# Kernel tuning notes

Measured on AMD Instinct MI355X. Metric: run time of the kernel, lower is better.

## Reference

```python
import jax, jax.numpy as jnp
import numpy as np

NHEAD = 4
HEAD_DIM = 64  # att_features per head = atten_feats // nhead


def setup_inputs() -> dict:
    key = jax.random.key(0)
    ks = jax.random.split(key, 8)
    N, D = 8192, 256
    s = 1.0 / np.sqrt(D)
    return {
        "x": jax.random.normal(ks[0], (N, D), dtype=jnp.float32),
        "edge": jax.random.randint(ks[1], (N, N), 0, 2, dtype=jnp.int32),
        "Wq": jax.random.normal(ks[2], (D, D), dtype=jnp.float32) * s,
        "bq": jax.random.normal(ks[3], (D,), dtype=jnp.float32) * 0.01,
        "Wk": jax.random.normal(ks[4], (D, D), dtype=jnp.float32) * s,
        "bk": jax.random.normal(ks[5], (D,), dtype=jnp.float32) * 0.01,
        "Wv": jax.random.normal(ks[6], (D, D), dtype=jnp.float32) * s,
        "bv": jax.random.normal(ks[7], (D,), dtype=jnp.float32) * 0.01,
    }


def _split_heads(t):
    # (N, H*d) -> (H, N, d)
    N = t.shape[0]
    return t.reshape(N, NHEAD, HEAD_DIM).transpose(1, 0, 2)


def reference(x, edge, Wq, bq, Wk, bk, Wv, bv):
    q = _split_heads(x @ Wq + bq)  # (H, N, d)
    k = _split_heads(x @ Wk + bk)
    v = _split_heads(x @ Wv + bv)
    # additive graph mask: 0 where edge.T == 1, -10000 where edge.T == 0
    mask = (edge.T.astype(jnp.float32) - 1.0) * 10000.0  # (N, N)
    scores = jnp.einsum("hnd,hmd->hnm", q, k) / np.sqrt(HEAD_DIM)
    scores = scores + mask[None, :, :]
    attn = jax.nn.softmax(scores, axis=-1)  # dropout is identity at eval
    ctx = jnp.einsum("hnm,hmd->hnd", attn, v)
    # (H, N, d) -> (N, H*d)
    return ctx.transpose(1, 0, 2).reshape(x.shape[0], NHEAD * HEAD_DIM)
```

## Files before the change

### kernel.cpp

```cpp
#include <hip/hip_runtime.h>
#include <stdint.h>

typedef unsigned short u16;
typedef unsigned int u32;
typedef unsigned long long u64;

typedef __attribute__((ext_vector_type(8))) __bf16 bf16x8;
typedef __attribute__((ext_vector_type(4))) float f32x4;

#define NROW 8192
#define DMODEL 256
#define HD 64
#define LDT 72

__device__ __forceinline__ u16 f2bf(float f) {
    u32 u = __builtin_bit_cast(u32, f);
    u += 0x7FFFu + ((u >> 16) & 1u);
    return (u16)(u >> 16);
}
__device__ __forceinline__ bf16x8 ldb8(const u16* p) {
    uint4 v = *(const uint4*)p;
    return __builtin_bit_cast(bf16x8, v);
}
__device__ __forceinline__ f32x4 mfma16(bf16x8 a, bf16x8 b, f32x4 c) {
    return __builtin_amdgcn_mfma_f32_16x16x32_bf16(a, b, c, 0, 0, 0);
}

__global__ __launch_bounds__(256) void k_prep(
    const float* __restrict__ x,
    const float* __restrict__ Wq, const float* __restrict__ Wk,
    const float* __restrict__ Wv,
    u16* __restrict__ xb, u16* __restrict__ Wt) {
    const int t = threadIdx.x;
    if (blockIdx.x < 1024) {
        size_t idx = (size_t)blockIdx.x * 2048 + t * 8;
        f32x4 a = *(const f32x4*)&x[idx];
        f32x4 b = *(const f32x4*)&x[idx + 4];
        uint4 o;
        o.x = (u32)f2bf(a[0]) | ((u32)f2bf(a[1]) << 16);
        o.y = (u32)f2bf(a[2]) | ((u32)f2bf(a[3]) << 16);
        o.z = (u32)f2bf(b[0]) | ((u32)f2bf(b[1]) << 16);
        o.w = (u32)f2bf(b[2]) | ((u32)f2bf(b[3]) << 16);
        *(uint4*)&xb[idx] = o;
        return;
    }
    __shared__ __align__(16) u16 lw[64 * LDT];
    int wb = blockIdx.x - 1024;
    int mat = wb >> 4, tile = wb & 15;
    int k0 = (tile >> 2) * 64, n0 = (tile & 3) * 64;
    const float* W = (mat == 0) ? Wq : ((mat == 1) ? Wk : Wv);
    #pragma unroll
    for (int i = 0; i < 4; ++i) {
        int c = t + 256 * i;
        int k = c >> 4, c4 = c & 15;
        f32x4 w4 = *(const f32x4*)&W[(size_t)(k0 + k) * DMODEL + n0 + c4 * 4];
        uint2 pk;
        pk.x = (u32)f2bf(w4[0]) | ((u32)f2bf(w4[1]) << 16);
        pk.y = (u32)f2bf(w4[2]) | ((u32)f2bf(w4[3]) << 16);
        *(uint2*)&lw[k * LDT + c4 * 4] = pk;
    }
    __syncthreads();
    #pragma unroll
    for (int i = 0; i < 2; ++i) {
        int c = t + 256 * i;
        int n = c >> 3, k8 = c & 7;
        union { uint4 u; u16 s[8]; } pk;
        #pragma unroll
        for (int j = 0; j < 8; ++j) pk.s[j] = lw[(k8 * 8 + j) * LDT + n];
        *(uint4*)&Wt[(size_t)mat * 65536 + (size_t)(n0 + n) * DMODEL + k0 + k8 * 8] = pk.u;
    }
}

__global__ __launch_bounds__(256) void k_bitmask(const int* __restrict__ edge,
                                                 u64* __restrict__ bits) {
    __shared__ u64 lb[8][128];
    const int t = threadIdx.x;
    const int lane = t & 63, w = t >> 6;
    const u32 m8 = blockIdx.x * 8u;
    #pragma unroll
    for (int rr = 0; rr < 2; ++rr) {
        const int mloc = w * 2 + rr;
        const size_t base = (size_t)(m8 + mloc) * NROW;
        for (int nwb = 0; nwb < 128; nwb += 16) {
            int v[16];
            #pragma unroll
            for (int j = 0; j < 16; ++j)
                v[j] = edge[base + (size_t)(nwb + j) * 64 + lane];
            u64 b[16];
            #pragma unroll
            for (int j = 0; j < 16; ++j) b[j] = __ballot(v[j] != 0);
            if (lane == 0) {
                #pragma unroll
                for (int j = 0; j < 16; ++j) lb[mloc][nwb + j] = b[j];
            }
        }
    }
    __syncthreads();
    const int nw = t >> 1, mh = (t & 1) * 4;
    u64 a0 = lb[mh + 0][nw], a1 = lb[mh + 1][nw];
    u64 a2 = lb[mh + 2][nw], a3 = lb[mh + 3][nw];
    u64* dst = &bits[(size_t)nw * NROW + m8 + mh];
    uint4 p0, p1;
    p0.x = (u32)a0; p0.y = (u32)(a0 >> 32); p0.z = (u32)a1; p0.w = (u32)(a1 >> 32);
    p1.x = (u32)a2; p1.y = (u32)(a2 >> 32); p1.z = (u32)a3; p1.w = (u32)(a3 >> 32);
    *(uint4*)dst = p0;
    *(uint4*)(dst + 2) = p1;
}

__global__ __launch_bounds__(256, 3) void k_qkv(
    const u16* __restrict__ xb, const u16* __restrict__ Wt,
    const float* __restrict__ bq, const float* __restrict__ bk,
    const float* __restrict__ bv,
    u16* __restrict__ Qo, u16* __restrict__ Ko, u16* __restrict__ Vt) {
    __shared__ __align__(16) u16 ax[128 * LDT];
    __shared__ __align__(16) u16 wt[64 * LDT];
    const int t = threadIdx.x;
    const int lane = t & 63, wv = t >> 6;
    const int q4 = lane >> 4, l15 = lane & 15;
    const int wr = wv >> 1, wc = wv & 1;
    const int row0 = blockIdx.x * 128;
    const int mat = blockIdx.y >> 2;
    const int c0 = (blockIdx.y & 3) * 64;
    const u16* Wm = Wt + (size_t)mat * 65536;
    const float* bias = (mat == 0) ? bq : ((mat == 1) ? bk : bv);

    f32x4 acc[8];
    #pragma unroll
    for (int i = 0; i < 8; ++i) acc[i] = {0.f, 0.f, 0.f, 0.f};

    for (int kk = 0; kk < DMODEL; kk += 64) {
        #pragma unroll
        for (int i = 0; i < 4; ++i) {
            int c = t + 256 * i;
            int row = c >> 3, c8 = c & 7;
            *(uint4*)&ax[row * LDT + c8 * 8] =
                *(const uint4*)&xb[(size_t)(row0 + row) * DMODEL + kk + c8 * 8];
        }
        #pragma unroll
        for (int i = 0; i < 2; ++i) {
            int c = t + 256 * i;
            int n = c >> 3, c8 = c & 7;
            *(uint4*)&wt[n * LDT + c8 * 8] =
                *(const uint4*)&Wm[(size_t)(c0 + n) * DMODEL + kk + c8 * 8];
        }
        __syncthreads();
        #pragma unroll
        for (int ks = 0; ks < 2; ++ks) {
            bf16x8 xf[4], wf[2];
            #pragma unroll
            for (int it = 0; it < 4; ++it)
                xf[it] = ldb8(&ax[(wr * 64 + it * 16 + l15) * LDT + ks * 32 + q4 * 8]);
            #pragma unroll
            for (int jt = 0; jt < 2; ++jt)
                wf[jt] = ldb8(&wt[(wc * 32 + jt * 16 + l15) * LDT + ks * 32 + q4 * 8]);
            if (mat < 2) {
                #pragma unroll
                for (int it = 0; it < 4; ++it)
                    #pragma unroll
                    for (int jt = 0; jt < 2; ++jt)
                        acc[it * 2 + jt] = mfma16(xf[it], wf[jt], acc[it * 2 + jt]);
            } else {
                #pragma unroll
                for (int jt = 0; jt < 2; ++jt)
                    #pragma unroll
                    for (int it = 0; it < 4; ++it)
                        acc[jt * 4 + it] = mfma16(wf[jt], xf[it], acc[jt * 4 + it]);
            }
        }
        __syncthreads();
    }

    if (mat < 2) {
        u16* out = (mat == 0) ? Qo : Ko;
        const float scale = (mat == 0) ? 0.18033688f : 1.0f;
        #pragma unroll
        for (int jt = 0; jt < 2; ++jt) {
            int col = c0 + wc * 32 + jt * 16 + l15;
            float bcol = bias[col];
            #pragma unroll
            for (int it = 0; it < 4; ++it) {
                int rowb = row0 + wr * 64 + it * 16 + q4 * 4;
                f32x4 a = acc[it * 2 + jt];
                #pragma unroll
                for (int r = 0; r < 4; ++r)
                    out[(size_t)(rowb + r) * DMODEL + col] = f2bf((a[r] + bcol) * scale);
            }
        }
    } else {
        #pragma unroll
        for (int jt = 0; jt < 2; ++jt) {
            #pragma unroll
            for (int r = 0; r < 4; ++r) {
                int drow = c0 + wc * 32 + jt * 16 + q4 * 4 + r;
                float bd = bias[drow];
                #pragma unroll
                for (int it = 0; it < 4; ++it) {
                    int col = row0 + wr * 64 + it * 16 + l15;
                    Vt[(size_t)drow * NROW + col] = f2bf(acc[jt * 4 + it][r] + bd);
                }
            }
        }
    }
}

__global__ __launch_bounds__(256, 2) void k_attn(
    const u16* __restrict__ Q, const u16* __restrict__ K,
    const u16* __restrict__ Vt, const u64* __restrict__ bits,
    float* __restrict__ po) {
    __shared__ __align__(16) u16 sK[2][64 * 64];
    __shared__ __align__(16) u16 sV[2][64 * 64];
    __shared__ __align__(16) u16 sP[4][16 * 64];
    __shared__ __align__(16) u32 sB[2][2][64];

    const int t = threadIdx.x;
    const int lane = t & 63, w = t >> 6;
    const int q4 = lane >> 4, l15 = lane & 15;
    const int l7 = l15 & 7;
    const int bid = blockIdx.x;
    const int sl = bid >> 9;
    const int b9 = bid & 511;
    const int h = (b9 >> 1) & 3;
    const int qt = ((b9 >> 3) << 1) | (b9 & 1);
    const int n0 = qt * 64;
    const int mbase = sl * 2048;
    const int half = w >> 1;
    const u32 shift = (u32)((w & 1) * 16 + l15);
    const int sr = t >> 3, sc = t & 7;
    const int ssw = (sc ^ (sr & 7)) * 8;

    bf16x8 qf[2];
    #pragma unroll
    for (int ks = 0; ks < 2; ++ks)
        qf[ks] = ldb8(&Q[(size_t)(n0 + w * 16 + l15) * DMODEL + h * HD + ks * 32 + q4 * 8]);

    uint4 onesu = {0x3F803F80u, 0x3F803F80u, 0x3F803F80u, 0x3F803F80u};
    const bf16x8 ones = __builtin_bit_cast(bf16x8, onesu);

    f32x4 o[4], lacc;
    lacc = {0.f, 0.f, 0.f, 0.f};
    #pragma unroll
    for (int dt = 0; dt < 4; ++dt) o[dt] = {0.f, 0.f, 0.f, 0.f};

    uint4 rk0, rk1, rv0, rv1; uint2 rb;
    {
        rk0 = *(const uint4*)&K[(size_t)(mbase + sr) * DMODEL + h * HD + sc * 8];
        rk1 = *(const uint4*)&K[(size_t)(mbase + 32 + sr) * DMODEL + h * HD + sc * 8];
        rv0 = *(const uint4*)&Vt[(size_t)(h * HD + sr) * NROW + mbase + sc * 8];
        rv1 = *(const uint4*)&Vt[(size_t)(h * HD + 32 + sr) * NROW + mbase + sc * 8];
        if (t < 64) rb = *(const uint2*)&bits[(size_t)qt * NROW + mbase + t];
        *(uint4*)&sK[0][sr * 64 + ssw] = rk0;
        *(uint4*)&sK[0][(32 + sr) * 64 + ssw] = rk1;
        *(uint4*)&sV[0][sr * 64 + ssw] = rv0;
        *(uint4*)&sV[0][(32 + sr) * 64 + ssw] = rv1;
        if (t < 64) { sB[0][0][t] = rb.x; sB[0][1][t] = rb.y; }
    }

    for (int it = 0; it < 32; ++it) {
        __syncthreads();
        const int buf = it & 1;
        if (it < 31) {
            int m0 = mbase + (it + 1) * 64;
            rk0 = *(const uint4*)&K[(size_t)(m0 + sr) * DMODEL + h * HD + sc * 8];
            rk1 = *(const uint4*)&K[(size_t)(m0 + 32 + sr) * DMODEL + h * HD + sc * 8];
            rv0 = *(const uint4*)&Vt[(size_t)(h * HD + sr) * NROW + m0 + sc * 8];
            rv1 = *(const uint4*)&Vt[(size_t)(h * HD + 32 + sr) * NROW + m0 + sc * 8];
            if (t < 64) rb = *(const uint2*)&bits[(size_t)qt * NROW + m0 + t];
        }

        f32x4 s[4];
        #pragma unroll
        for (int tj = 0; tj < 4; ++tj) s[tj] = {0.f, 0.f, 0.f, 0.f};
        #pragma unroll
        for (int ks = 0; ks < 2; ++ks) {
            bf16x8 kb[4];
            #pragma unroll
            for (int tj = 0; tj < 4; ++tj)
                kb[tj] = ldb8(&sK[buf][(tj * 16 + l15) * 64 + (((ks * 4 + q4) ^ l7) * 8)]);
            #pragma unroll
            for (int tj = 0; tj < 4; ++tj)
                s[tj] = mfma16(kb[tj], qf[ks], s[tj]);
        }

        #pragma unroll
        for (int tj = 0; tj < 4; ++tj) {
            uint4 bw = *(const uint4*)&sB[buf][half][tj * 16 + q4 * 4];
            u32 wd[4] = {bw.x, bw.y, bw.z, bw.w};
            u32 ub[4];
            #pragma unroll
            for (int r = 0; r < 4; ++r) {
                float sv = ((wd[r] >> shift) & 1u) ? s[tj][r] : -1e30f;
                ub[r] = __builtin_bit_cast(u32, __builtin_amdgcn_exp2f(sv));
            }
            uint2 pk;
            pk.x = (ub[0] >> 16) | (ub[1] & 0xFFFF0000u);
            pk.y = (ub[2] >> 16) | (ub[3] & 0xFFFF0000u);
            *(uint2*)&sP[w][l15 * 64 + (((tj * 2 + (q4 >> 1)) ^ l7) * 8) + (q4 & 1) * 4] = pk;
        }
        asm volatile("s_waitcnt lgkmcnt(0)" ::: "memory");

        #pragma unroll
        for (int ks = 0; ks < 2; ++ks) {
            bf16x8 pf = ldb8(&sP[w][l15 * 64 + (((ks * 4 + q4) ^ l7) * 8)]);
            bf16x8 vb[4];
            #pragma unroll
            for (int dt = 0; dt < 4; ++dt)
                vb[dt] = ldb8(&sV[buf][(dt * 16 + l15) * 64 + (((ks * 4 + q4) ^ l7) * 8)]);
            #pragma unroll
            for (int dt = 0; dt < 4; ++dt)
                o[dt] = mfma16(pf, vb[dt], o[dt]);
            lacc = mfma16(pf, ones, lacc);
        }

        if (it < 31) {
            const int nb = buf ^ 1;
            *(uint4*)&sK[nb][sr * 64 + ssw] = rk0;
            *(uint4*)&sK[nb][(32 + sr) * 64 + ssw] = rk1;
            *(uint4*)&sV[nb][sr * 64 + ssw] = rv0;
            *(uint4*)&sV[nb][(32 + sr) * 64 + ssw] = rv1;
            if (t < 64) { sB[nb][0][t] = rb.x; sB[nb][1][t] = rb.y; }
        }
    }

    float* pob = po + (size_t)bid * 4160;
    #pragma unroll
    for (int dt = 0; dt < 4; ++dt)
        *(f32x4*)&pob[(dt * 16 + l15) * 64 + w * 16 + q4 * 4] = o[dt];
    if (l15 == 0) {
        #pragma unroll
        for (int r = 0; r < 4; ++r) pob[4096 + w * 16 + q4 * 4 + r] = lacc[r];
    }
}

__global__ __launch_bounds__(256) void k_reduce(const float* __restrict__ po,
                                                float* __restrict__ out) {
    __shared__ float sT[64 * 68];
    __shared__ float sL[64];
    const int t = threadIdx.x;
    const int b9 = blockIdx.x;
    const int h = (b9 >> 1) & 3;
    const int qt = ((b9 >> 3) << 1) | (b9 & 1);
    const int n0 = qt * 64;
    const size_t base = (size_t)b9 * 4160;
    const int d = t >> 2, ng = (t & 3) * 16;
    f32x4 a[4];
    #pragma unroll
    for (int j = 0; j < 4; ++j) a[j] = {0.f, 0.f, 0.f, 0.f};
    #pragma unroll
    for (int s = 0; s < 4; ++s) {
        const float* p = po + base + (size_t)s * (512 * 4160) + d * 64 + ng;
        #pragma unroll
        for (int j = 0; j < 4; ++j) a[j] += *(const f32x4*)&p[j * 4];
    }
    #pragma unroll
    for (int j = 0; j < 4; ++j) *(f32x4*)&sT[d * 68 + ng + j * 4] = a[j];
    if (t < 64) {
        float l = 0.f;
        #pragma unroll
        for (int s = 0; s < 4; ++s) l += po[base + (size_t)s * (512 * 4160) + 4096 + t];
        sL[t] = l;
    }
    __syncthreads();
    const int n = t >> 2, dg = (t & 3) * 16;
    float inv = __builtin_amdgcn_rcpf(sL[n] + 1e-30f);
    #pragma unroll
    for (int j = 0; j < 4; ++j) {
        f32x4 v;
        #pragma unroll
        for (int i = 0; i < 4; ++i) v[i] = sT[(dg + j * 4 + i) * 68 + n];
        v = v * inv;
        *(f32x4*)&out[(size_t)(n0 + n) * DMODEL + h * HD + dg + j * 4] = v;
    }
}

extern "C" void kernel_launch(void* const* d_in, const int* in_sizes, int n_in,
                              void* d_out, int out_size, void* d_ws, size_t ws_size,
                              hipStream_t stream) {
    const float* x  = (const float*)d_in[0];
    const int* edge = (const int*)d_in[1];
    const float* Wq = (const float*)d_in[2];
    const float* bq = (const float*)d_in[3];
    const float* Wk = (const float*)d_in[4];
    const float* bk = (const float*)d_in[5];
    const float* Wv = (const float*)d_in[6];
    const float* bv = (const float*)d_in[7];

    char* ws = (char*)d_ws;
    u64* bits = (u64*)ws;
    u16* Qo  = (u16*)(ws + (8u << 20));
    u16* Ko  = (u16*)(ws + (12u << 20));
    u16* Vt  = (u16*)(ws + (16u << 20));
    u16* xb  = (u16*)(ws + (20u << 20));
    u16* Wt  = (u16*)(ws + (24u << 20));
    float* po = (float*)(ws + (32u << 20));
    float* out = (float*)d_out;

    hipLaunchKernelGGL(k_prep, dim3(1072), dim3(256), 0, stream, x, Wq, Wk, Wv, xb, Wt);
    hipLaunchKernelGGL(k_bitmask, dim3(1024), dim3(256), 0, stream, edge, bits);
    hipLaunchKernelGGL(k_qkv, dim3(64, 12), dim3(256), 0, stream,
                       xb, Wt, bq, bk, bv, Qo, Ko, Vt);
    hipLaunchKernelGGL(k_attn, dim3(2048), dim3(256), 0, stream, Qo, Ko, Vt, bits, po);
    hipLaunchKernelGGL(k_reduce, dim3(512), dim3(256), 0, stream, po, out);
}
```

Before: 514.4 us.

## Process two query tiles per attention block to reuse K/V tiles

Each attention block now handles 128 query rows (two 64-row tiles) per head and key slice, so every K and V tile staged in shared memory feeds twice as many MFMAs. The grid drops to 1024 attention blocks and 256 reduce blocks, and the partial-output layout and reduce kernel are adapted to match. The aim is to halve K/V global and LDS traffic per unit of work. In exchange it roughly doubles accumulator and score registers and enlarges the P buffer in shared memory, which may limit occupancy even with launch bounds raised to 3.

```diff
diff --git a/kernel.cpp b/kernel.cpp
--- a/kernel.cpp
+++ b/kernel.cpp
@@ -203,43 +203,50 @@
     }
 }
 
-__global__ __launch_bounds__(256, 2) void k_attn(
+__global__ __launch_bounds__(256, 3) void k_attn(
     const u16* __restrict__ Q, const u16* __restrict__ K,
     const u16* __restrict__ Vt, const u64* __restrict__ bits,
     float* __restrict__ po) {
     __shared__ __align__(16) u16 sK[2][64 * 64];
     __shared__ __align__(16) u16 sV[2][64 * 64];
-    __shared__ __align__(16) u16 sP[4][16 * 64];
-    __shared__ __align__(16) u32 sB[2][2][64];
+    __shared__ __align__(16) u16 sP[4][32 * 64];
+    __shared__ __align__(16) u32 sB[2][2][2][64];
 
     const int t = threadIdx.x;
     const int lane = t & 63, w = t >> 6;
     const int q4 = lane >> 4, l15 = lane & 15;
     const int l7 = l15 & 7;
     const int bid = blockIdx.x;
-    const int sl = bid >> 9;
-    const int b9 = bid & 511;
-    const int h = (b9 >> 1) & 3;
-    const int qt = ((b9 >> 3) << 1) | (b9 & 1);
-    const int n0 = qt * 64;
+    const int sl = bid >> 8;
+    const int b8 = bid & 255;
+    const int h = b8 & 3;
+    const int qt = b8 >> 2;
+    const int n0 = qt * 128;
     const int mbase = sl * 2048;
     const int half = w >> 1;
     const u32 shift = (u32)((w & 1) * 16 + l15);
     const int sr = t >> 3, sc = t & 7;
     const int ssw = (sc ^ (sr & 7)) * 8;
-
-    bf16x8 qf[2];
-    #pragma unroll
-    for (int ks = 0; ks < 2; ++ks)
-        qf[ks] = ldb8(&Q[(size_t)(n0 + w * 16 + l15) * DMODEL + h * HD + ks * 32 + q4 * 8]);
+    const int bg = t >> 6, bm = t & 63;
+
+    bf16x8 qf[2][2];
+    #pragma unroll
+    for (int nt = 0; nt < 2; ++nt)
+        #pragma unroll
+        for (int ks = 0; ks < 2; ++ks)
+            qf[nt][ks] = ldb8(&Q[(size_t)(n0 + nt * 64 + w * 16 + l15) * DMODEL +
+                                 h * HD + ks * 32 + q4 * 8]);
 
     uint4 onesu = {0x3F803F80u, 0x3F803F80u, 0x3F803F80u, 0x3F803F80u};
     const bf16x8 ones = __builtin_bit_cast(bf16x8, onesu);
 
-    f32x4 o[4], lacc;
-    lacc = {0.f, 0.f, 0.f, 0.f};
-    #pragma unroll
-    for (int dt = 0; dt < 4; ++dt) o[dt] = {0.f, 0.f, 0.f, 0.f};
+    f32x4 o[2][4], lacc[2];
+    #pragma unroll
+    for (int nt = 0; nt < 2; ++nt) {
+        lacc[nt] = {0.f, 0.f, 0.f, 0.f};
+        #pragma unroll
+        for (int dt = 0; dt < 4; ++dt) o[nt][dt] = {0.f, 0.f, 0.f, 0.f};
+    }
 
     uint4 rk0, rk1, rv0, rv1; uint2 rb;
     {
@@ -247,12 +254,12 @@
         rk1 = *(const uint4*)&K[(size_t)(mbase + 32 + sr) * DMODEL + h * HD + sc * 8];
         rv0 = *(const uint4*)&Vt[(size_t)(h * HD + sr) * NROW + mbase + sc * 8];
         rv1 = *(const uint4*)&Vt[(size_t)(h * HD + 32 + sr) * NROW + mbase + sc * 8];
-        if (t < 64) rb = *(const uint2*)&bits[(size_t)qt * NROW + mbase + t];
+        if (t < 128) rb = *(const uint2*)&bits[(size_t)(qt * 2 + bg) * NROW + mbase + bm];
         *(uint4*)&sK[0][sr * 64 + ssw] = rk0;
         *(uint4*)&sK[0][(32 + sr) * 64 + ssw] = rk1;
         *(uint4*)&sV[0][sr * 64 + ssw] = rv0;
         *(uint4*)&sV[0][(32 + sr) * 64 + ssw] = rv1;
-        if (t < 64) { sB[0][0][t] = rb.x; sB[0][1][t] = rb.y; }
+        if (t < 128) { sB[0][bg][0][bm] = rb.x; sB[0][bg][1][bm] = rb.y; }
     }
 
     for (int it = 0; it < 32; ++it) {
@@ -264,12 +271,14 @@
             rk1 = *(const uint4*)&K[(size_t)(m0 + 32 + sr) * DMODEL + h * HD + sc * 8];
             rv0 = *(const uint4*)&Vt[(size_t)(h * HD + sr) * NROW + m0 + sc * 8];
             rv1 = *(const uint4*)&Vt[(size_t)(h * HD + 32 + sr) * NROW + m0 + sc * 8];
-            if (t < 64) rb = *(const uint2*)&bits[(size_t)qt * NROW + m0 + t];
-        }
-
-        f32x4 s[4];
-        #pragma unroll
-        for (int tj = 0; tj < 4; ++tj) s[tj] = {0.f, 0.f, 0.f, 0.f};
+            if (t < 128) rb = *(const uint2*)&bits[(size_t)(qt * 2 + bg) * NROW + m0 + bm];
+        }
+
+        f32x4 s[2][4];
+        #pragma unroll
+        for (int nt = 0; nt < 2; ++nt)
+            #pragma unroll
+            for (int tj = 0; tj < 4; ++tj) s[nt][tj] = {0.f, 0.f, 0.f, 0.f};
         #pragma unroll
         for (int ks = 0; ks < 2; ++ks) {
             bf16x8 kb[4];
@@ -277,38 +286,49 @@
             for (int tj = 0; tj < 4; ++tj)
                 kb[tj] = ldb8(&sK[buf][(tj * 16 + l15) * 64 + (((ks * 4 + q4) ^ l7) * 8)]);
             #pragma unroll
-            for (int tj = 0; tj < 4; ++tj)
-                s[tj] = mfma16(kb[tj], qf[ks], s[tj]);
-        }
-
-        #pragma unroll
-        for (int tj = 0; tj < 4; ++tj) {
-            uint4 bw = *(const uint4*)&sB[buf][half][tj * 16 + q4 * 4];
-            u32 wd[4] = {bw.x, bw.y, bw.z, bw.w};
-            u32 ub[4];
-            #pragma unroll
-            for (int r = 0; r < 4; ++r) {
-                float sv = ((wd[r] >> shift) & 1u) ? s[tj][r] : -1e30f;
-                ub[r] = __builtin_bit_cast(u32, __builtin_amdgcn_exp2f(sv));
-            }
-            uint2 pk;
-            pk.x = (ub[0] >> 16) | (ub[1] & 0xFFFF0000u);
-            pk.y = (ub[2] >> 16) | (ub[3] & 0xFFFF0000u);
-            *(uint2*)&sP[w][l15 * 64 + (((tj * 2 + (q4 >> 1)) ^ l7) * 8) + (q4 & 1) * 4] = pk;
+            for (int nt = 0; nt < 2; ++nt)
+                #pragma unroll
+                for (int tj = 0; tj < 4; ++tj)
+                    s[nt][tj] = mfma16(kb[tj], qf[nt][ks], s[nt][tj]);
+        }
+
+        #pragma unroll
+        for (int nt = 0; nt < 2; ++nt) {
+            #pragma unroll
+            for (int tj = 0; tj < 4; ++tj) {
+                uint4 bw = *(const uint4*)&sB[buf][nt][half][tj * 16 + q4 * 4];
+                u32 wd[4] = {bw.x, bw.y, bw.z, bw.w};
+                u32 ub[4];
+                #pragma unroll
+                for (int r = 0; r < 4; ++r) {
+                    float sv = ((wd[r] >> shift) & 1u) ? s[nt][tj][r] : -1e30f;
+                    ub[r] = __builtin_bit_cast(u32, __builtin_amdgcn_exp2f(sv));
+                }
+                uint2 pk;
+                pk.x = (ub[0] >> 16) | (ub[1] & 0xFFFF0000u);
+                pk.y = (ub[2] >> 16) | (ub[3] & 0xFFFF0000u);
+                *(uint2*)&sP[w][(nt * 16 + l15) * 64 +
+                                (((tj * 2 + (q4 >> 1)) ^ l7) * 8) + (q4 & 1) * 4] = pk;
+            }
         }
         asm volatile("s_waitcnt lgkmcnt(0)" ::: "memory");
 
         #pragma unroll
         for (int ks = 0; ks < 2; ++ks) {
-            bf16x8 pf = ldb8(&sP[w][l15 * 64 + (((ks * 4 + q4) ^ l7) * 8)]);
-            bf16x8 vb[4];
+            bf16x8 pf[2], vb[4];
+            #pragma unroll
+            for (int nt = 0; nt < 2; ++nt)
+                pf[nt] = ldb8(&sP[w][(nt * 16 + l15) * 64 + (((ks * 4 + q4) ^ l7) * 8)]);
             #pragma unroll
             for (int dt = 0; dt < 4; ++dt)
                 vb[dt] = ldb8(&sV[buf][(dt * 16 + l15) * 64 + (((ks * 4 + q4) ^ l7) * 8)]);
             #pragma unroll
-            for (int dt = 0; dt < 4; ++dt)
-                o[dt] = mfma16(pf, vb[dt], o[dt]);
-            lacc = mfma16(pf, ones, lacc);
+            for (int nt = 0; nt < 2; ++nt) {
+                #pragma unroll
+                for (int dt = 0; dt < 4; ++dt)
+                    o[nt][dt] = mfma16(pf[nt], vb[dt], o[nt][dt]);
+                lacc[nt] = mfma16(pf[nt], ones, lacc[nt]);
+            }
         }
 
         if (it < 31) {
@@ -317,56 +337,61 @@
             *(uint4*)&sK[nb][(32 + sr) * 64 + ssw] = rk1;
             *(uint4*)&sV[nb][sr * 64 + ssw] = rv0;
             *(uint4*)&sV[nb][(32 + sr) * 64 + ssw] = rv1;
-            if (t < 64) { sB[nb][0][t] = rb.x; sB[nb][1][t] = rb.y; }
-        }
-    }
-
-    float* pob = po + (size_t)bid * 4160;
-    #pragma unroll
-    for (int dt = 0; dt < 4; ++dt)
-        *(f32x4*)&pob[(dt * 16 + l15) * 64 + w * 16 + q4 * 4] = o[dt];
+            if (t < 128) { sB[nb][bg][0][bm] = rb.x; sB[nb][bg][1][bm] = rb.y; }
+        }
+    }
+
+    float* pob = po + (size_t)bid * 8320;
+    #pragma unroll
+    for (int nt = 0; nt < 2; ++nt)
+        #pragma unroll
+        for (int dt = 0; dt < 4; ++dt)
+            *(f32x4*)&pob[(dt * 16 + l15) * 128 + nt * 64 + w * 16 + q4 * 4] = o[nt][dt];
     if (l15 == 0) {
         #pragma unroll
-        for (int r = 0; r < 4; ++r) pob[4096 + w * 16 + q4 * 4 + r] = lacc[r];
+        for (int nt = 0; nt < 2; ++nt)
+            #pragma unroll
+            for (int r = 0; r < 4; ++r)
+                pob[8192 + nt * 64 + w * 16 + q4 * 4 + r] = lacc[nt][r];
     }
 }
 
 __global__ __launch_bounds__(256) void k_reduce(const float* __restrict__ po,
                                                 float* __restrict__ out) {
-    __shared__ float sT[64 * 68];
-    __shared__ float sL[64];
+    __shared__ float sT[64 * 132];
+    __shared__ float sL[128];
     const int t = threadIdx.x;
-    const int b9 = blockIdx.x;
-    const int h = (b9 >> 1) & 3;
-    const int qt = ((b9 >> 3) << 1) | (b9 & 1);
-    const int n0 = qt * 64;
-    const size_t base = (size_t)b9 * 4160;
-    const int d = t >> 2, ng = (t & 3) * 16;
-    f32x4 a[4];
-    #pragma unroll
-    for (int j = 0; j < 4; ++j) a[j] = {0.f, 0.f, 0.f, 0.f};
+    const int b8 = blockIdx.x;
+    const int h = b8 & 3;
+    const int qt = b8 >> 2;
+    const int n0 = qt * 128;
+    const size_t base = (size_t)b8 * 8320;
+    const int d = t >> 2, ng = (t & 3) * 32;
+    f32x4 a[8];
+    #pragma unroll
+    for (int j = 0; j < 8; ++j) a[j] = {0.f, 0.f, 0.f, 0.f};
     #pragma unroll
     for (int s = 0; s < 4; ++s) {
-        const float* p = po + base + (size_t)s * (512 * 4160) + d * 64 + ng;
-        #pragma unroll
-        for (int j = 0; j < 4; ++j) a[j] += *(const f32x4*)&p[j * 4];
-    }
-    #pragma unroll
-    for (int j = 0; j < 4; ++j) *(f32x4*)&sT[d * 68 + ng + j * 4] = a[j];
-    if (t < 64) {
+        const float* p = po + base + (size_t)s * (256 * 8320) + d * 128 + ng;
+        #pragma unroll
+        for (int j = 0; j < 8; ++j) a[j] += *(const f32x4*)&p[j * 4];
+    }
+    #pragma unroll
+    for (int j = 0; j < 8; ++j) *(f32x4*)&sT[d * 132 + ng + j * 4] = a[j];
+    if (t < 128) {
         float l = 0.f;
         #pragma unroll
-        for (int s = 0; s < 4; ++s) l += po[base + (size_t)s * (512 * 4160) + 4096 + t];
+        for (int s = 0; s < 4; ++s) l += po[base + (size_t)s * (256 * 8320) + 8192 + t];
         sL[t] = l;
     }
     __syncthreads();
-    const int n = t >> 2, dg = (t & 3) * 16;
+    const int n = t >> 1, dg = (t & 1) * 32;
     float inv = __builtin_amdgcn_rcpf(sL[n] + 1e-30f);
     #pragma unroll
-    for (int j = 0; j < 4; ++j) {
+    for (int j = 0; j < 8; ++j) {
         f32x4 v;
         #pragma unroll
-        for (int i = 0; i < 4; ++i) v[i] = sT[(dg + j * 4 + i) * 68 + n];
+        for (int i = 0; i < 4; ++i) v[i] = sT[(dg + j * 4 + i) * 132 + n];
         v = v * inv;
         *(f32x4*)&out[(size_t)(n0 + n) * DMODEL + h * HD + dg + j * 4] = v;
     }
@@ -398,6 +423,6 @@
     hipLaunchKernelGGL(k_bitmask, dim3(1024), dim3(256), 0, stream, edge, bits);
     hipLaunchKernelGGL(k_qkv, dim3(64, 12), dim3(256), 0, stream,
                        xb, Wt, bq, bk, bv, Qo, Ko, Vt);
-    hipLaunchKernelGGL(k_attn, dim3(2048), dim3(256), 0, stream, Qo, Ko, Vt, bits, po);
-    hipLaunchKernelGGL(k_reduce, dim3(512), dim3(256), 0, stream, po, out);
-}
+    hipLaunchKernelGGL(k_attn, dim3(1024), dim3(256), 0, stream, Qo, Ko, Vt, bits, po);
+    hipLaunchKernelGGL(k_reduce, dim3(256), dim3(256), 0, stream, po, out);
+}
```

Result: faster. 503.4 us (-2.1%).
